# Optimization experiments

Measured on AMD Instinct MI355X. Metric: run time of the kernel, lower is better.

The kernel has to match this reference:

```python
import jax, jax.numpy as jnp
import numpy as np
from jax import lax

C64 = jnp.complex64
N_WIRES = 4
BSZ, IMH, IMW = 1024, 64, 64

# --- deterministic RandomLayer spec: 50 ops from {rx,ry,rz,crx} (stands in for tq.RandomLayer RNG) ---
_rng = np.random.RandomState(42)
RAND_OPS = []
for _ in range(50):
    g = int(_rng.randint(4))
    if g < 3:
        RAND_OPS.append((g, (int(_rng.randint(N_WIRES)),)))
    else:
        w = _rng.choice(N_WIRES, 2, replace=False)
        RAND_OPS.append((g, (int(w[0]), int(w[1]))))

def _c(x):
    return x.astype(C64)

def rx_mat(t):
    c, s = _c(jnp.cos(t / 2)), _c(jnp.sin(t / 2))
    return jnp.stack([jnp.stack([c, -1j * s], -1), jnp.stack([-1j * s, c], -1)], -2)

def ry_mat(t):
    c, s = _c(jnp.cos(t / 2)), _c(jnp.sin(t / 2))
    return jnp.stack([jnp.stack([c, -s], -1), jnp.stack([s, c], -1)], -2)

def rz_mat(t):
    e0 = jnp.exp(-1j * _c(t) / 2)
    e1 = jnp.exp(1j * _c(t) / 2)
    z = jnp.zeros_like(e0)
    return jnp.stack([jnp.stack([e0, z], -1), jnp.stack([z, e1], -1)], -2)

def crx_mat(t):
    # control = first wire (|1> block gets RX)
    return jnp.eye(4, dtype=C64).at[2:, 2:].set(rx_mat(t))

H_MAT = jnp.array([[1, 1], [1, -1]], dtype=C64) / np.sqrt(2.0)
SX_MAT = 0.5 * jnp.array([[1 + 1j, 1 - 1j], [1 - 1j, 1 + 1j]], dtype=C64)
CNOT_MAT = jnp.array([[1, 0, 0, 0], [0, 1, 0, 0], [0, 0, 0, 1], [0, 0, 1, 0]], dtype=C64)

def apply_1q(state, U, wire):
    # state: (b,2,2,2,2) with wire 0 = most significant axis; U: (2,2) or (b,2,2)
    s = jnp.moveaxis(state, wire + 1, -1)
    shp = s.shape
    s = s.reshape(shp[0], -1, 2)
    if U.ndim == 2:
        s = jnp.einsum('ij,bkj->bki', U, s)
    else:
        s = jnp.einsum('bij,bkj->bki', U, s)
    return jnp.moveaxis(s.reshape(shp), -1, wire + 1)

def apply_2q(state, U, w0, w1):
    # U: (4,4), row/col index = 2*bit(w0) + bit(w1)
    s = jnp.moveaxis(state, (w0 + 1, w1 + 1), (-2, -1))
    shp = s.shape
    s = s.reshape(shp[0], -1, 4)
    s = jnp.einsum('ij,bkj->bki', U, s)
    return jnp.moveaxis(s.reshape(shp), (-2, -1), (w0 + 1, w1 + 1))

def _conv(x, w, b):
    y = lax.conv_general_dilated(x, w, (1, 1), 'SAME', dimension_numbers=('NCHW', 'OIHW', 'NCHW'))
    return y + b[None, :, None, None]

def _maxpool2(x):
    return lax.reduce_window(x, -jnp.inf, lax.max, (1, 1, 2, 2), (1, 1, 2, 2), 'VALID')

ENC_FUNCS = [ry_mat, rz_mat, rx_mat, ry_mat]  # tq encoder '4x4_ryzxy'

def _forward(x, conv1_w, conv1_b, conv2_w, conv2_b, rl_params, q_params,
             head_w, head_b, bn_gamma, bn_beta, bn_mean, bn_var):
    b = x.shape[0]
    h = _maxpool2(jax.nn.relu(_conv(x, conv1_w, conv1_b)))
    h = _maxpool2(jax.nn.relu(_conv(h, conv2_w, conv2_b)))
    pooled = h.mean(axis=(2, 3))  # (b,16) global avg pool
    state = jnp.zeros((b, 16), dtype=C64).at[:, 0].set(1.0).reshape(b, 2, 2, 2, 2)
    # GeneralEncoder '4x4_ryzxy': 16 batched single-qubit rotations
    idx = 0
    for mf in ENC_FUNCS:
        for w in range(N_WIRES):
            state = apply_1q(state, mf(pooled[:, idx]), w)
            idx += 1
    # RandomLayer (deterministic spec, trainable angles)
    rot = {0: rx_mat, 1: ry_mat, 2: rz_mat}
    for i, (g, wires) in enumerate(RAND_OPS):
        t = rl_params[i]
        if g < 3:
            state = apply_1q(state, rot[g](t), wires[0])
        else:
            state = apply_2q(state, crx_mat(t), wires[0], wires[1])
    # fixed trainable gates: rx0@0, ry0@1, rz0@3, crx0@[0,2], H@3, SX@2, CNOT@[3,0]
    state = apply_1q(state, rx_mat(q_params[0]), 0)
    state = apply_1q(state, ry_mat(q_params[1]), 1)
    state = apply_1q(state, rz_mat(q_params[2]), 3)
    state = apply_2q(state, crx_mat(q_params[3]), 0, 2)
    state = apply_1q(state, H_MAT, 3)
    state = apply_1q(state, SX_MAT, 2)
    state = apply_2q(state, CNOT_MAT, 3, 0)
    # MeasureAll(PauliZ): <Z_w> per wire
    probs = state.real ** 2 + state.imag ** 2  # (b,2,2,2,2)
    z = jnp.array([1.0, -1.0], dtype=probs.dtype)
    feats = jnp.stack(
        [jnp.sum(probs * z.reshape([1] + [2 if a == w else 1 for a in range(4)]),
                 axis=(1, 2, 3, 4)) for w in range(N_WIRES)], axis=-1)  # (b,4)
    out = feats @ head_w.T + head_b  # (b,1)
    out = bn_gamma * (out - bn_mean) / jnp.sqrt(bn_var + 1e-5) + bn_beta  # BN eval mode
    return out.squeeze(-1)

def setup_inputs() -> dict:
    key = jax.random.key(0)
    ks = jax.random.split(key, 8)
    return {
        'x': jax.random.normal(ks[0], (BSZ, 1, IMH, IMW), jnp.float32),
        'conv1_w': jax.random.normal(ks[1], (8, 1, 3, 3), jnp.float32) * 0.2,
        'conv1_b': jnp.zeros((8,), jnp.float32),
        'conv2_w': jax.random.normal(ks[2], (16, 8, 3, 3), jnp.float32) * 0.1,
        'conv2_b': jnp.zeros((16,), jnp.float32),
        'rl_params': jax.random.uniform(ks[3], (50,), jnp.float32, 0.0, 2 * np.pi),
        'q_params': jax.random.uniform(ks[4], (4,), jnp.float32, 0.0, 2 * np.pi),
        'head_w': jax.random.normal(ks[5], (1, 4), jnp.float32) * 0.5,
        'head_b': jnp.zeros((1,), jnp.float32),
        'bn_gamma': jnp.ones((1,), jnp.float32),
        'bn_beta': jnp.zeros((1,), jnp.float32),
        'bn_mean': jnp.zeros((1,), jnp.float32),
        'bn_var': jnp.ones((1,), jnp.float32),
    }

def reference(x, conv1_w, conv1_b, conv2_w, conv2_b, rl_params, q_params,
              head_w, head_b, bn_gamma, bn_beta, bn_mean, bn_var):
    return _forward(x, conv1_w, conv1_b, conv2_w, conv2_b, rl_params, q_params,
                    head_w, head_b, bn_gamma, bn_beta, bn_mean, bn_var)
```

## Files before the change

kernel.cpp:

```cpp
#include <hip/hip_runtime.h>
#include <math.h>

__device__ __forceinline__ float2 cmul(float2 a, float2 b) {
    return make_float2(a.x * b.x - a.y * b.y, a.x * b.y + a.y * b.x);
}
__device__ __forceinline__ float2 cadd(float2 a, float2 b) {
    return make_float2(a.x + b.x, a.y + b.y);
}

struct CxOps { int ty[57]; int wa[57]; int wb[57]; };

constexpr CxOps cx_gen() {
    CxOps S{};
    unsigned mt[624] = {};
    mt[0] = 42u;
    for (int i = 1; i < 624; ++i)
        mt[i] = 1812433253u * (mt[i - 1] ^ (mt[i - 1] >> 30)) + (unsigned)i;
    int mti = 624;
    auto nextu = [&]() constexpr -> unsigned {
        if (mti >= 624) {
            for (int i = 0; i < 624; ++i) {
                unsigned y = (mt[i] & 0x80000000u) | (mt[(i + 1) % 624] & 0x7fffffffu);
                mt[i] = mt[(i + 397) % 624] ^ (y >> 1) ^ ((y & 1u) ? 2567483615u : 0u);
            }
            mti = 0;
        }
        unsigned y = mt[mti++];
        y ^= y >> 11;
        y ^= (y << 7)  & 2636928640u;
        y ^= (y << 15) & 4022730752u;
        y ^= y >> 18;
        return y;
    };
    for (int k = 0; k < 50; ++k) {
        unsigned g = nextu() & 3u;
        if (g < 3u) {
            unsigned w = nextu() & 3u;
            S.ty[k] = (int)g; S.wa[k] = (int)w; S.wb[k] = 0;
        } else {
            int arr[4] = {0, 1, 2, 3};
            unsigned j3 = nextu() & 3u;
            { int tmp = arr[3]; arr[3] = arr[j3]; arr[j3] = tmp; }
            unsigned j2 = nextu() & 3u;
            while (j2 > 2u) j2 = nextu() & 3u;
            { int tmp = arr[2]; arr[2] = arr[j2]; arr[j2] = tmp; }
            unsigned j1 = nextu() & 1u;
            { int tmp = arr[1]; arr[1] = arr[j1]; arr[j1] = tmp; }
            S.ty[k] = 3; S.wa[k] = arr[0]; S.wb[k] = arr[1];
        }
    }
    S.ty[50] = 0; S.wa[50] = 0; S.wb[50] = 0;
    S.ty[51] = 1; S.wa[51] = 1; S.wb[51] = 0;
    S.ty[52] = 2; S.wa[52] = 3; S.wb[52] = 0;
    S.ty[53] = 3; S.wa[53] = 0; S.wb[53] = 2;
    S.ty[54] = 4; S.wa[54] = 3; S.wb[54] = 0;
    S.ty[55] = 5; S.wa[55] = 2; S.wb[55] = 0;
    S.ty[56] = 6; S.wa[56] = 3; S.wb[56] = 0;
    return S;
}
constexpr CxOps C_OPS = cx_gen();

struct CxMeta { int cm[57]; int tm[57]; };
constexpr CxMeta cx_meta_gen() {
    CxMeta M{};
    for (int k = 0; k < 57; ++k) {
        int ty = C_OPS.ty[k];
        if (ty == 3 || ty == 6) { M.cm[k] = 8 >> C_OPS.wa[k]; M.tm[k] = 8 >> C_OPS.wb[k]; }
        else                    { M.cm[k] = 0;               M.tm[k] = 8 >> C_OPS.wa[k]; }
    }
    return M;
}
constexpr CxMeta C_META = cx_meta_gen();

__device__ __forceinline__ void unitary_body(const float* __restrict__ rl,
                                             const float* __restrict__ qp,
                                             float2* __restrict__ Uout,
                                             float2 (&mats)[57][4], float2 (&buf)[2][256])
{
    const int t = threadIdx.x;
    const int r = t >> 4, c = t & 15;

    if (t < 57) {
        const int ty = C_OPS.ty[t];
        const float th = (t < 50) ? rl[t] : ((t < 54) ? qp[t - 50] : 0.f);
        float sh, ch;
        sincosf(0.5f * th, &sh, &ch);
        float2 m00, m01, m10, m11;
        if (ty == 0 || ty == 3) {
            m00 = make_float2(ch, 0.f); m01 = make_float2(0.f, -sh);
            m10 = make_float2(0.f, -sh); m11 = make_float2(ch, 0.f);
        } else if (ty == 1) {
            m00 = make_float2(ch, 0.f); m01 = make_float2(-sh, 0.f);
            m10 = make_float2(sh, 0.f); m11 = make_float2(ch, 0.f);
        } else if (ty == 2) {
            m00 = make_float2(ch, -sh); m01 = make_float2(0.f, 0.f);
            m10 = make_float2(0.f, 0.f); m11 = make_float2(ch, sh);
        } else if (ty == 4) {
            const float r_ = 0.70710678118654752f;
            m00 = make_float2(r_, 0.f); m01 = make_float2(r_, 0.f);
            m10 = make_float2(r_, 0.f); m11 = make_float2(-r_, 0.f);
        } else if (ty == 5) {
            m00 = make_float2(0.5f, 0.5f);  m01 = make_float2(0.5f, -0.5f);
            m10 = make_float2(0.5f, -0.5f); m11 = make_float2(0.5f, 0.5f);
        } else {
            m00 = make_float2(0.f, 0.f); m01 = make_float2(1.f, 0.f);
            m10 = make_float2(1.f, 0.f); m11 = make_float2(0.f, 0.f);
        }
        mats[t][0] = m00; mats[t][1] = m01; mats[t][2] = m10; mats[t][3] = m11;
    }
    buf[0][t] = make_float2((r == c) ? 1.f : 0.f, 0.f);
    __syncthreads();

    int p = 0;
    #pragma unroll 1
    for (int k = 0; k < 57; ++k) {
        const int cm = C_META.cm[k], tm = C_META.tm[k];
        const float2 m00 = mats[k][0], m01 = mats[k][1];
        const float2 m10 = mats[k][2], m11 = mats[k][3];
        const float2 me = buf[p][t];
        const float2 pv = buf[p][(r ^ tm) * 16 + c];
        float2 nv;
        if (r & tm) nv = cadd(cmul(m10, pv), cmul(m11, me));
        else        nv = cadd(cmul(m00, me), cmul(m01, pv));
        if ((r & cm) != cm) nv = me;
        buf[p ^ 1][t] = nv;
        __syncthreads();
        p ^= 1;
    }
    Uout[t] = buf[p][t];
}

__global__ __launch_bounds__(256)
void unitary_lds_kernel(const float* __restrict__ rl, const float* __restrict__ qp,
                        float2* __restrict__ Uout)
{
    __shared__ float2 mats[57][4];
    __shared__ float2 buf[2][256];
    unitary_body(rl, qp, Uout, mats, buf);
}

__global__ __launch_bounds__(256, 4)
void conv1_kernel(const float* __restrict__ X, const float* __restrict__ W1,
                  const float* __restrict__ B1, float* __restrict__ h1g,
                  const float* __restrict__ rl, const float* __restrict__ qp,
                  float2* __restrict__ Uout)
{
    const int bx = blockIdx.x, t = threadIdx.x;
    __shared__ float xin[34 * 66];

    if (bx == 2048) {
        __shared__ float2 mats[57][4];
        __shared__ float2 buf[2][256];
        unitary_body(rl, qp, Uout, mats, buf);
        return;
    }

    const int b = bx >> 1, h = bx & 1;
    const float* xb = X + (size_t)b * 4096;
    const int rbase = 32 * h - 1;
    for (int idx = t; idx < 34 * 66; idx += 256) {
        int ly = idx / 66, lx = idx - ly * 66;
        int gy = rbase + ly, gx = lx - 1;
        float v = 0.f;
        if (gy >= 0 && gy < 64 && gx >= 0 && gx < 64) v = xb[gy * 64 + gx];
        xin[idx] = v;
    }
    __syncthreads();

    #pragma unroll
    for (int j = 0; j < 2; ++j) {
        const int cell = t + 256 * j;
        const int py = cell >> 5, px = cell & 31;
        const int base = (2 * py) * 66 + 2 * px;
        float win[4][4];
        #pragma unroll
        for (int r = 0; r < 4; ++r) {
            float2 p0 = *(const float2*)&xin[base + r * 66];
            float2 p1 = *(const float2*)&xin[base + r * 66 + 2];
            win[r][0] = p0.x; win[r][1] = p0.y; win[r][2] = p1.x; win[r][3] = p1.y;
        }
        const int gcell = (16 * h + py) * 32 + px;
        #pragma unroll
        for (int g = 0; g < 2; ++g) {
            float acc[4][4];
            #pragma unroll
            for (int o = 0; o < 4; ++o) {
                float bb = B1[g * 4 + o];
                acc[o][0] = bb; acc[o][1] = bb; acc[o][2] = bb; acc[o][3] = bb;
            }
            #pragma unroll
            for (int o = 0; o < 4; ++o) {
                const float* wp = W1 + (g * 4 + o) * 9;
                #pragma unroll
                for (int ky = 0; ky < 3; ++ky)
                    #pragma unroll
                    for (int kx = 0; kx < 3; ++kx) {
                        float w = wp[ky * 3 + kx];
                        acc[o][0] = fmaf(win[ky][kx],         w, acc[o][0]);
                        acc[o][1] = fmaf(win[ky][kx + 1],     w, acc[o][1]);
                        acc[o][2] = fmaf(win[ky + 1][kx],     w, acc[o][2]);
                        acc[o][3] = fmaf(win[ky + 1][kx + 1], w, acc[o][3]);
                    }
            }
            #pragma unroll
            for (int o = 0; o < 4; ++o) {
                float m = fmaxf(fmaxf(acc[o][0], acc[o][1]), fmaxf(acc[o][2], acc[o][3]));
                h1g[((size_t)b * 8 + g * 4 + o) * 1024 + gcell] = fmaxf(m, 0.f);
            }
        }
    }
}

__global__ __launch_bounds__(256, 4)
void conv2_head_kernel(const float* __restrict__ h1g, const float* __restrict__ W2,
                       const float* __restrict__ B2, const float2* __restrict__ Ug,
                       const float* __restrict__ head_w, const float* __restrict__ head_b,
                       const float* __restrict__ bn_g, const float* __restrict__ bn_b,
                       const float* __restrict__ bn_m, const float* __restrict__ bn_v,
                       float* __restrict__ out)
{
    const int b = blockIdx.x, t = threadIdx.x;
    __shared__ float h1s[8 * 34 * 34];
    __shared__ float2 Ul[256];
    __shared__ float red[16 * 4];
    __shared__ float pool16[16];

    Ul[t] = Ug[t];
    for (int i = t; i < 8 * 34 * 34; i += 256) h1s[i] = 0.f;
    __syncthreads();
    {
        const float4* src = (const float4*)(h1g + (size_t)b * 8192);
        #pragma unroll
        for (int k = 0; k < 8; ++k) {
            const int i4 = t + k * 256;
            const float4 v = src[i4];
            const int oc = i4 >> 8, c4 = i4 & 255;
            const int y = c4 >> 3, xq = (c4 & 7) << 2;
            const int base = oc * 1156 + (y + 1) * 34 + (xq + 1);
            h1s[base + 0] = v.x; h1s[base + 1] = v.y;
            h1s[base + 2] = v.z; h1s[base + 3] = v.w;
        }
    }
    __syncthreads();

    const int py = t >> 4, px = t & 15;
    const int y0 = 2 * py, x0 = 2 * px;
    const int lane = t & 63, wid = t >> 6;

    float acc[16][4];
    #pragma unroll
    for (int o = 0; o < 16; ++o) {
        float bb = B2[o];
        acc[o][0] = bb; acc[o][1] = bb; acc[o][2] = bb; acc[o][3] = bb;
    }
    #pragma unroll 1
    for (int ic = 0; ic < 8; ++ic) {
        const int base = ic * 1156 + y0 * 34 + x0;
        float win[4][4];
        #pragma unroll
        for (int r = 0; r < 4; ++r) {
            float2 p0 = *(const float2*)&h1s[base + r * 34];
            float2 p1 = *(const float2*)&h1s[base + r * 34 + 2];
            win[r][0] = p0.x; win[r][1] = p0.y; win[r][2] = p1.x; win[r][3] = p1.y;
        }
        #pragma unroll
        for (int o = 0; o < 16; ++o) {
            const float* wp = W2 + (size_t)(o * 8 + ic) * 9;
            #pragma unroll
            for (int ky = 0; ky < 3; ++ky)
                #pragma unroll
                for (int kx = 0; kx < 3; ++kx) {
                    float w = wp[ky * 3 + kx];
                    acc[o][0] = fmaf(win[ky][kx],         w, acc[o][0]);
                    acc[o][1] = fmaf(win[ky][kx + 1],     w, acc[o][1]);
                    acc[o][2] = fmaf(win[ky + 1][kx],     w, acc[o][2]);
                    acc[o][3] = fmaf(win[ky + 1][kx + 1], w, acc[o][3]);
                }
        }
    }
    #pragma unroll
    for (int o = 0; o < 16; ++o) {
        float m = fmaxf(fmaxf(acc[o][0], acc[o][1]), fmaxf(acc[o][2], acc[o][3]));
        float v = fmaxf(m, 0.f);
        #pragma unroll
        for (int off = 32; off > 0; off >>= 1)
            v += __shfl_down(v, off, 64);
        if (lane == 0) red[o * 4 + wid] = v;
    }
    __syncthreads();
    if (t < 16)
        pool16[t] = (red[t * 4] + red[t * 4 + 1] + red[t * 4 + 2] + red[t * 4 + 3]) * (1.0f / 256.0f);
    __syncthreads();

    if (t < 16) {
        float2 v0[4], v1[4];
        #pragma unroll
        for (int w = 0; w < 4; ++w) {
            float a  = pool16[w];
            float bz = pool16[4 + w];
            float gx = pool16[8 + w];
            float dl = pool16[12 + w];
            float sa, ca, sb, cb, sg, cg, sd, cd;
            sincosf(0.5f * a,  &sa, &ca);
            sincosf(0.5f * bz, &sb, &cb);
            sincosf(0.5f * gx, &sg, &cg);
            sincosf(0.5f * dl, &sd, &cd);
            float2 u0 = make_float2(ca * cb, -ca * sb);
            float2 u1 = make_float2(sa * cb,  sa * sb);
            float2 w0 = make_float2(cg * u0.x + sg * u1.y, cg * u0.y - sg * u1.x);
            float2 w1 = make_float2(sg * u0.y + cg * u1.x, -sg * u0.x + cg * u1.y);
            v0[w] = make_float2(cd * w0.x - sd * w1.x, cd * w0.y - sd * w1.y);
            v1[w] = make_float2(sd * w0.x + cd * w1.x, sd * w0.y + cd * w1.y);
        }
        float2 s01[4], s23[4];
        s01[0] = cmul(v0[0], v0[1]); s01[1] = cmul(v0[0], v1[1]);
        s01[2] = cmul(v1[0], v0[1]); s01[3] = cmul(v1[0], v1[1]);
        s23[0] = cmul(v0[2], v0[3]); s23[1] = cmul(v0[2], v1[3]);
        s23[2] = cmul(v1[2], v0[3]); s23[3] = cmul(v1[2], v1[3]);
        float2 acc2 = make_float2(0.f, 0.f);
        #pragma unroll
        for (int i = 0; i < 4; ++i)
            #pragma unroll
            for (int j = 0; j < 4; ++j) {
                float2 sij = cmul(s01[i], s23[j]);
                acc2 = cadd(acc2, cmul(Ul[t * 16 + i * 4 + j], sij));
            }
        float pr = acc2.x * acc2.x + acc2.y * acc2.y;
        float fz0 = 0.f, fz1 = 0.f, fz2 = 0.f, fz3 = 0.f;
        #pragma unroll
        for (int i = 0; i < 16; ++i) {
            float p = __shfl(pr, i, 64);
            fz0 += ((i >> 3) & 1) ? -p : p;
            fz1 += ((i >> 2) & 1) ? -p : p;
            fz2 += ((i >> 1) & 1) ? -p : p;
            fz3 += (i & 1) ? -p : p;
        }
        if (t == 0) {
            float o = head_b[0];
            o = fmaf(fz0, head_w[0], o);
            o = fmaf(fz1, head_w[1], o);
            o = fmaf(fz2, head_w[2], o);
            o = fmaf(fz3, head_w[3], o);
            o = bn_g[0] * (o - bn_m[0]) / sqrtf(bn_v[0] + 1e-5f) + bn_b[0];
            out[b] = o;
        }
    }
}

__global__ __launch_bounds__(256, 2)
void fused_cnn_kernel(const float* __restrict__ X,
                      const float* __restrict__ W1, const float* __restrict__ B1,
                      const float* __restrict__ W2, const float* __restrict__ B2,
                      float* __restrict__ pooled)
{
    const int b = blockIdx.x;
    const int t = threadIdx.x;
    __shared__ float xin[66 * 66];
    __shared__ float h1[8 * 34 * 34];
    __shared__ float red[16 * 4];

    const float* xb = X + (size_t)b * (64 * 64);
    for (int idx = t; idx < 66 * 66; idx += 256) {
        int y = idx / 66, x = idx - y * 66;
        float v = 0.f;
        if (y >= 1 && y <= 64 && x >= 1 && x <= 64)
            v = xb[(y - 1) * 64 + (x - 1)];
        xin[idx] = v;
    }
    for (int idx = t; idx < 8 * 34 * 34; idx += 256) h1[idx] = 0.f;
    __syncthreads();

    for (int cell = t; cell < 1024; cell += 256) {
        int py = cell >> 5, px = cell & 31;
        int y0 = 2 * py, x0 = 2 * px;
        float win[4][4];
        #pragma unroll
        for (int r = 0; r < 4; ++r)
            #pragma unroll
            for (int c = 0; c < 4; ++c)
                win[r][c] = xin[(y0 + r) * 66 + (x0 + c)];
        #pragma unroll
        for (int oc = 0; oc < 8; ++oc) {
            float bb = B1[oc];
            float a00 = bb, a01 = bb, a10 = bb, a11 = bb;
            #pragma unroll
            for (int ky = 0; ky < 3; ++ky)
                #pragma unroll
                for (int kx = 0; kx < 3; ++kx) {
                    float w = W1[oc * 9 + ky * 3 + kx];
                    a00 = fmaf(win[ky][kx],         w, a00);
                    a01 = fmaf(win[ky][kx + 1],     w, a01);
                    a10 = fmaf(win[ky + 1][kx],     w, a10);
                    a11 = fmaf(win[ky + 1][kx + 1], w, a11);
                }
            float m = fmaxf(fmaxf(a00, a01), fmaxf(a10, a11));
            h1[oc * (34 * 34) + (py + 1) * 34 + (px + 1)] = fmaxf(m, 0.f);
        }
    }
    __syncthreads();

    const int py = t >> 4, px = t & 15;
    const int y0 = 2 * py, x0 = 2 * px;
    const int lane = t & 63, wid = t >> 6;

    for (int g = 0; g < 4; ++g) {
        float acc[4][4];
        #pragma unroll
        for (int o = 0; o < 4; ++o) {
            float bb = B2[g * 4 + o];
            acc[o][0] = bb; acc[o][1] = bb; acc[o][2] = bb; acc[o][3] = bb;
        }
        for (int ic = 0; ic < 8; ++ic) {
            float win[4][4];
            #pragma unroll
            for (int r = 0; r < 4; ++r)
                #pragma unroll
                for (int c = 0; c < 4; ++c)
                    win[r][c] = h1[ic * (34 * 34) + (y0 + r) * 34 + (x0 + c)];
            #pragma unroll
            for (int o = 0; o < 4; ++o) {
                const float* wp = W2 + (size_t)(g * 4 + o) * 72 + ic * 9;
                #pragma unroll
                for (int ky = 0; ky < 3; ++ky)
                    #pragma unroll
                    for (int kx = 0; kx < 3; ++kx) {
                        float w = wp[ky * 3 + kx];
                        acc[o][0] = fmaf(win[ky][kx],         w, acc[o][0]);
                        acc[o][1] = fmaf(win[ky][kx + 1],     w, acc[o][1]);
                        acc[o][2] = fmaf(win[ky + 1][kx],     w, acc[o][2]);
                        acc[o][3] = fmaf(win[ky + 1][kx + 1], w, acc[o][3]);
                    }
            }
        }
        #pragma unroll
        for (int o = 0; o < 4; ++o) {
            float m = fmaxf(fmaxf(acc[o][0], acc[o][1]), fmaxf(acc[o][2], acc[o][3]));
            float v = fmaxf(m, 0.f);
            #pragma unroll
            for (int off = 32; off > 0; off >>= 1)
                v += __shfl_down(v, off, 64);
            if (lane == 0) red[(g * 4 + o) * 4 + wid] = v;
        }
    }
    __syncthreads();
    if (t < 16) {
        float s = red[t * 4] + red[t * 4 + 1] + red[t * 4 + 2] + red[t * 4 + 3];
        pooled[(size_t)b * 16 + t] = s * (1.0f / 256.0f);
    }
}

__global__ __launch_bounds__(256)
void quantum_head_kernel(const float* __restrict__ pooled, const float2* __restrict__ Uin,
                         const float* __restrict__ head_w, const float* __restrict__ head_b,
                         const float* __restrict__ bn_g, const float* __restrict__ bn_b,
                         const float* __restrict__ bn_m, const float* __restrict__ bn_v,
                         float* __restrict__ out)
{
    __shared__ float2 U[256];
    const int t = threadIdx.x;
    U[t] = Uin[t];
    __syncthreads();
    const int b = blockIdx.x * 256 + t;

    float2 v0[4], v1[4];
    #pragma unroll
    for (int w = 0; w < 4; ++w) {
        float a  = pooled[(size_t)b * 16 + w];
        float bz = pooled[(size_t)b * 16 + 4 + w];
        float gx = pooled[(size_t)b * 16 + 8 + w];
        float dl = pooled[(size_t)b * 16 + 12 + w];
        float sa, ca, sb, cb, sg, cg, sd, cd;
        sincosf(0.5f * a,  &sa, &ca);
        sincosf(0.5f * bz, &sb, &cb);
        sincosf(0.5f * gx, &sg, &cg);
        sincosf(0.5f * dl, &sd, &cd);
        float2 u0 = make_float2(ca * cb, -ca * sb);
        float2 u1 = make_float2(sa * cb,  sa * sb);
        float2 w0 = make_float2(cg * u0.x + sg * u1.y, cg * u0.y - sg * u1.x);
        float2 w1 = make_float2(sg * u0.y + cg * u1.x, -sg * u0.x + cg * u1.y);
        v0[w] = make_float2(cd * w0.x - sd * w1.x, cd * w0.y - sd * w1.y);
        v1[w] = make_float2(sd * w0.x + cd * w1.x, sd * w0.y + cd * w1.y);
    }
    float2 s01[4], s23[4], s[16];
    s01[0] = cmul(v0[0], v0[1]); s01[1] = cmul(v0[0], v1[1]);
    s01[2] = cmul(v1[0], v0[1]); s01[3] = cmul(v1[0], v1[1]);
    s23[0] = cmul(v0[2], v0[3]); s23[1] = cmul(v0[2], v1[3]);
    s23[2] = cmul(v1[2], v0[3]); s23[3] = cmul(v1[2], v1[3]);
    #pragma unroll
    for (int i = 0; i < 4; ++i)
        #pragma unroll
        for (int j = 0; j < 4; ++j)
            s[i * 4 + j] = cmul(s01[i], s23[j]);

    float fz0 = 0.f, fz1 = 0.f, fz2 = 0.f, fz3 = 0.f;
    #pragma unroll
    for (int i = 0; i < 16; ++i) {
        float2 acc = make_float2(0.f, 0.f);
        #pragma unroll
        for (int j = 0; j < 16; ++j)
            acc = cadd(acc, cmul(U[i * 16 + j], s[j]));
        float pr = acc.x * acc.x + acc.y * acc.y;
        fz0 += ((i >> 3) & 1) ? -pr : pr;
        fz1 += ((i >> 2) & 1) ? -pr : pr;
        fz2 += ((i >> 1) & 1) ? -pr : pr;
        fz3 += (i & 1) ? -pr : pr;
    }
    float o = head_b[0];
    o = fmaf(fz0, head_w[0], o);
    o = fmaf(fz1, head_w[1], o);
    o = fmaf(fz2, head_w[2], o);
    o = fmaf(fz3, head_w[3], o);
    o = bn_g[0] * (o - bn_m[0]) / sqrtf(bn_v[0] + 1e-5f) + bn_b[0];
    out[b] = o;
}

extern "C" void kernel_launch(void* const* d_in, const int* in_sizes, int n_in,
                              void* d_out, int out_size, void* d_ws, size_t ws_size,
                              hipStream_t stream)
{
    const float* X  = (const float*)d_in[0];
    const float* W1 = (const float*)d_in[1];
    const float* B1 = (const float*)d_in[2];
    const float* W2 = (const float*)d_in[3];
    const float* B2 = (const float*)d_in[4];
    const float* RL = (const float*)d_in[5];
    const float* QP = (const float*)d_in[6];
    const float* HW = (const float*)d_in[7];
    const float* HB = (const float*)d_in[8];
    const float* BG = (const float*)d_in[9];
    const float* BB = (const float*)d_in[10];
    const float* BM = (const float*)d_in[11];
    const float* BV = (const float*)d_in[12];
    float* out = (float*)d_out;

    const size_t H1_BYTES = (size_t)1024 * 8 * 1024 * 4;

    if (ws_size >= H1_BYTES + 4096) {
        float*  h1g = (float*)d_ws;
        float2* U   = (float2*)((char*)d_ws + H1_BYTES);
        conv1_kernel<<<2049, 256, 0, stream>>>(X, W1, B1, h1g, RL, QP, U);
        conv2_head_kernel<<<1024, 256, 0, stream>>>(h1g, W2, B2, U,
                                                    HW, HB, BG, BB, BM, BV, out);
    } else {
        float*  pooled = (float*)d_ws;
        float2* U      = (float2*)((char*)d_ws + 1024 * 16 * 4);
        unitary_lds_kernel<<<1, 256, 0, stream>>>(RL, QP, U);
        fused_cnn_kernel<<<1024, 256, 0, stream>>>(X, W1, B1, W2, B2, pooled);
        quantum_head_kernel<<<4, 256, 0, stream>>>(pooled, U, HW, HB, BG, BB, BM, BV, out);
    }
}
```

Baseline: 75.62 us.

## Split conv2-head per image across two blocks with atomic last-block reduction

The conv2+head kernel now launches two blocks per image, each handling half the rows (16 output rows plus halo). Threads are split into two groups of eight output channels, so each thread's accumulator array shrinks from 16 to 8 channels. Partial pooled sums go to global memory, and an atomic counter picks the last-arriving block to run the quantum head. The aim is more parallelism, lower register pressure and a smaller shared-memory footprint for higher occupancy. In exchange it adds a memset launch, atomics and reloading of halo rows.

```diff
diff --git a/kernel.cpp b/kernel.cpp
--- a/kernel.cpp
+++ b/kernel.cpp
@@ -212,50 +212,56 @@
 }
 
 __global__ __launch_bounds__(256, 4)
-void conv2_head_kernel(const float* __restrict__ h1g, const float* __restrict__ W2,
-                       const float* __restrict__ B2, const float2* __restrict__ Ug,
-                       const float* __restrict__ head_w, const float* __restrict__ head_b,
-                       const float* __restrict__ bn_g, const float* __restrict__ bn_b,
-                       const float* __restrict__ bn_m, const float* __restrict__ bn_v,
-                       float* __restrict__ out)
-{
-    const int b = blockIdx.x, t = threadIdx.x;
-    __shared__ float h1s[8 * 34 * 34];
-    __shared__ float2 Ul[256];
-    __shared__ float red[16 * 4];
-    __shared__ float pool16[16];
-
-    Ul[t] = Ug[t];
-    for (int i = t; i < 8 * 34 * 34; i += 256) h1s[i] = 0.f;
-    __syncthreads();
+void conv2h_kernel(const float* __restrict__ h1g, const float* __restrict__ W2,
+                   const float* __restrict__ B2, const float2* __restrict__ Ug,
+                   const float* __restrict__ head_w, const float* __restrict__ head_b,
+                   const float* __restrict__ bn_g, const float* __restrict__ bn_b,
+                   const float* __restrict__ bn_m, const float* __restrict__ bn_v,
+                   float* __restrict__ part, int* __restrict__ cnt,
+                   float* __restrict__ out)
+{
+    const int bx = blockIdx.x, t = threadIdx.x;
+    const int b = bx >> 1, hr = bx & 1;
+    __shared__ float h1s[8 * 18 * 34];
+    __shared__ float red[16 * 2];
+    __shared__ int winner;
+
+    for (int i = t; i < 8 * 18; i += 256) {
+        int ic = i / 18, row = i - ic * 18;
+        h1s[ic * 612 + row * 34 + 0]  = 0.f;
+        h1s[ic * 612 + row * 34 + 33] = 0.f;
+    }
     {
         const float4* src = (const float4*)(h1g + (size_t)b * 8192);
-        #pragma unroll
-        for (int k = 0; k < 8; ++k) {
-            const int i4 = t + k * 256;
-            const float4 v = src[i4];
-            const int oc = i4 >> 8, c4 = i4 & 255;
-            const int y = c4 >> 3, xq = (c4 & 7) << 2;
-            const int base = oc * 1156 + (y + 1) * 34 + (xq + 1);
+        const int grb = hr * 16 - 1;
+        for (int i4 = t; i4 < 1152; i4 += 256) {
+            const int oc = i4 / 144, rem = i4 - oc * 144;
+            const int row = rem >> 3, c4 = rem & 7;
+            const int gr = grb + row;
+            float4 v = make_float4(0.f, 0.f, 0.f, 0.f);
+            if (gr >= 0 && gr < 32) v = src[(oc * 1024 + gr * 32 + c4 * 4) >> 2];
+            const int base = oc * 612 + row * 34 + c4 * 4 + 1;
             h1s[base + 0] = v.x; h1s[base + 1] = v.y;
             h1s[base + 2] = v.z; h1s[base + 3] = v.w;
         }
     }
     __syncthreads();
 
-    const int py = t >> 4, px = t & 15;
-    const int y0 = 2 * py, x0 = 2 * px;
-    const int lane = t & 63, wid = t >> 6;
-
-    float acc[16][4];
+    const int cell = t & 127;
+    const int ocg  = t >> 7;
+    const int p  = cell >> 4, px = cell & 15;
+    const int lbase = (2 * p) * 34 + 2 * px;
+    const int w2 = t >> 6;
+
+    float acc[8][4];
     #pragma unroll
-    for (int o = 0; o < 16; ++o) {
-        float bb = B2[o];
+    for (int o = 0; o < 8; ++o) {
+        float bb = B2[ocg * 8 + o];
         acc[o][0] = bb; acc[o][1] = bb; acc[o][2] = bb; acc[o][3] = bb;
     }
     #pragma unroll 1
     for (int ic = 0; ic < 8; ++ic) {
-        const int base = ic * 1156 + y0 * 34 + x0;
+        const int base = ic * 612 + lbase;
         float win[4][4];
         #pragma unroll
         for (int r = 0; r < 4; ++r) {
@@ -264,8 +270,8 @@
             win[r][0] = p0.x; win[r][1] = p0.y; win[r][2] = p1.x; win[r][3] = p1.y;
         }
         #pragma unroll
-        for (int o = 0; o < 16; ++o) {
-            const float* wp = W2 + (size_t)(o * 8 + ic) * 9;
+        for (int o = 0; o < 8; ++o) {
+            const float* wp = W2 + (size_t)((ocg * 8 + o) * 8 + ic) * 9;
             #pragma unroll
             for (int ky = 0; ky < 3; ++ky)
                 #pragma unroll
@@ -279,27 +285,42 @@
         }
     }
     #pragma unroll
-    for (int o = 0; o < 16; ++o) {
+    for (int o = 0; o < 8; ++o) {
         float m = fmaxf(fmaxf(acc[o][0], acc[o][1]), fmaxf(acc[o][2], acc[o][3]));
         float v = fmaxf(m, 0.f);
         #pragma unroll
         for (int off = 32; off > 0; off >>= 1)
             v += __shfl_down(v, off, 64);
-        if (lane == 0) red[o * 4 + wid] = v;
-    }
-    __syncthreads();
-    if (t < 16)
-        pool16[t] = (red[t * 4] + red[t * 4 + 1] + red[t * 4 + 2] + red[t * 4 + 3]) * (1.0f / 256.0f);
-    __syncthreads();
-
+        if ((t & 63) == 0) red[(ocg * 8 + o) * 2 + (w2 & 1)] = v;
+    }
+    __syncthreads();
     if (t < 16) {
+        float s = red[t * 2] + red[t * 2 + 1];
+        __hip_atomic_store(&part[((size_t)b * 2 + hr) * 16 + t], s,
+                           __ATOMIC_RELEASE, __HIP_MEMORY_SCOPE_AGENT);
+    }
+    __syncthreads();
+    if (t == 0) {
+        int old = __hip_atomic_fetch_add(&cnt[b], 1, __ATOMIC_ACQ_REL,
+                                         __HIP_MEMORY_SCOPE_AGENT);
+        winner = (old == 1);
+    }
+    __syncthreads();
+    if (!winner) return;
+
+    if (t < 16) {
+        float pa = __hip_atomic_load(&part[((size_t)b * 2 + 0) * 16 + t],
+                                     __ATOMIC_ACQUIRE, __HIP_MEMORY_SCOPE_AGENT);
+        float pb = __hip_atomic_load(&part[((size_t)b * 2 + 1) * 16 + t],
+                                     __ATOMIC_ACQUIRE, __HIP_MEMORY_SCOPE_AGENT);
+        float pl = (pa + pb) * (1.0f / 256.0f);
         float2 v0[4], v1[4];
         #pragma unroll
         for (int w = 0; w < 4; ++w) {
-            float a  = pool16[w];
-            float bz = pool16[4 + w];
-            float gx = pool16[8 + w];
-            float dl = pool16[12 + w];
+            float a  = __shfl(pl, w, 64);
+            float bz = __shfl(pl, 4 + w, 64);
+            float gx = __shfl(pl, 8 + w, 64);
+            float dl = __shfl(pl, 12 + w, 64);
             float sa, ca, sb, cb, sg, cg, sd, cd;
             sincosf(0.5f * a,  &sa, &ca);
             sincosf(0.5f * bz, &sb, &cb);
@@ -323,17 +344,17 @@
             #pragma unroll
             for (int j = 0; j < 4; ++j) {
                 float2 sij = cmul(s01[i], s23[j]);
-                acc2 = cadd(acc2, cmul(Ul[t * 16 + i * 4 + j], sij));
+                acc2 = cadd(acc2, cmul(Ug[t * 16 + i * 4 + j], sij));
             }
         float pr = acc2.x * acc2.x + acc2.y * acc2.y;
         float fz0 = 0.f, fz1 = 0.f, fz2 = 0.f, fz3 = 0.f;
         #pragma unroll
         for (int i = 0; i < 16; ++i) {
-            float p = __shfl(pr, i, 64);
-            fz0 += ((i >> 3) & 1) ? -p : p;
-            fz1 += ((i >> 2) & 1) ? -p : p;
-            fz2 += ((i >> 1) & 1) ? -p : p;
-            fz3 += (i & 1) ? -p : p;
+            float pp = __shfl(pr, i, 64);
+            fz0 += ((i >> 3) & 1) ? -pp : pp;
+            fz1 += ((i >> 2) & 1) ? -pp : pp;
+            fz2 += ((i >> 1) & 1) ? -pp : pp;
+            fz3 += (i & 1) ? -pp : pp;
         }
         if (t == 0) {
             float o = head_b[0];
@@ -533,14 +554,20 @@
     const float* BV = (const float*)d_in[12];
     float* out = (float*)d_out;
 
-    const size_t H1_BYTES = (size_t)1024 * 8 * 1024 * 4;
-
-    if (ws_size >= H1_BYTES + 4096) {
-        float*  h1g = (float*)d_ws;
-        float2* U   = (float2*)((char*)d_ws + H1_BYTES);
+    const size_t H1_BYTES   = (size_t)1024 * 8 * 1024 * 4;
+    const size_t U_BYTES    = 4096;
+    const size_t PART_BYTES = (size_t)1024 * 2 * 16 * 4;
+    const size_t CNT_BYTES  = (size_t)1024 * 4;
+
+    if (ws_size >= H1_BYTES + U_BYTES + PART_BYTES + CNT_BYTES) {
+        float*  h1g  = (float*)d_ws;
+        float2* U    = (float2*)((char*)d_ws + H1_BYTES);
+        float*  part = (float*)((char*)d_ws + H1_BYTES + U_BYTES);
+        int*    cnt  = (int*)((char*)d_ws + H1_BYTES + U_BYTES + PART_BYTES);
+        hipMemsetAsync(cnt, 0, CNT_BYTES, stream);
         conv1_kernel<<<2049, 256, 0, stream>>>(X, W1, B1, h1g, RL, QP, U);
-        conv2_head_kernel<<<1024, 256, 0, stream>>>(h1g, W2, B2, U,
-                                                    HW, HB, BG, BB, BM, BV, out);
+        conv2h_kernel<<<2048, 256, 0, stream>>>(h1g, W2, B2, U,
+                                                HW, HB, BG, BB, BM, BV, part, cnt, out);
     } else {
         float*  pooled = (float*)d_ws;
         float2* U      = (float2*)((char*)d_ws + 1024 * 16 * 4);
```

After: 155.6 us. 106% more time.
